# Kernel optimization log

Hardware: AMD Instinct MI355X
Metric: run time of the kernel (lower is better)

Reference implementation:

```python
import jax, jax.numpy as jnp
import numpy as np

TAU = 2.0
V_TH = 1.0
V_RESET = 0.0
BN_EPS = 1e-5
SG_ALPHA = 2.0  # spikingjelly ATan surrogate default

@jax.custom_vjp
def spike_fn(x):
    return (x >= 0.0).astype(x.dtype)

def _spike_fwd(x):
    return spike_fn(x), x

def _spike_bwd(x, g):
    # ATan surrogate: alpha/2 / (1 + (pi/2*alpha*x)^2)
    sg = (SG_ALPHA / 2.0) / (1.0 + (jnp.pi / 2.0 * SG_ALPHA * x) ** 2)
    return (g * sg,)

spike_fn.defvjp(_spike_fwd, _spike_bwd)

def lif_multistep(x_seq):
    # x_seq: [T, B, C]; decay_input=False, hard reset, detach_reset=True
    def step(v, xt):
        v = v - (v - V_RESET) / TAU + xt
        s = spike_fn(v - V_TH)
        sd = jax.lax.stop_gradient(s)
        v = (1.0 - sd) * v + sd * V_RESET
        return v, s
    v0 = jnp.zeros_like(x_seq[0])
    _, s_seq = jax.lax.scan(step, v0, x_seq)
    return s_seq

def bn_eval(x, gamma, beta, mean, var):
    # x: [T, B, C], normalize over channel C (eval-mode BN)
    inv = gamma * jax.lax.rsqrt(var + BN_EPS)
    return x * inv + (beta - mean * inv)

def setup_inputs() -> dict:
    key = jax.random.key(0)
    ks = jax.random.split(key, 8)
    B, T, Cin, C, K = 64, 200, 80, 1024, 7
    x = jax.random.normal(ks[0], (B, T, Cin), dtype=jnp.float32)
    pw_w = jax.random.normal(ks[1], (C, Cin), dtype=jnp.float32) * (1.0 / np.sqrt(Cin))
    pw_b = jnp.zeros((C,), dtype=jnp.float32)
    dw_w = jax.random.normal(ks[2], (C, K), dtype=jnp.float32) * (1.0 / np.sqrt(K))
    dw_b = jnp.zeros((C,), dtype=jnp.float32)
    bn1_gamma = jnp.ones((C,), dtype=jnp.float32)
    bn1_beta = jnp.zeros((C,), dtype=jnp.float32)
    bn1_mean = jnp.zeros((C,), dtype=jnp.float32)
    bn1_var = jnp.ones((C,), dtype=jnp.float32)
    lin_w = jax.random.normal(ks[3], (C, C), dtype=jnp.float32) * (1.0 / np.sqrt(C))
    bn2_gamma = jnp.ones((C,), dtype=jnp.float32)
    bn2_beta = jnp.zeros((C,), dtype=jnp.float32)
    bn2_mean = jnp.zeros((C,), dtype=jnp.float32)
    bn2_var = jnp.ones((C,), dtype=jnp.float32)
    return dict(x=x, pw_w=pw_w, pw_b=pw_b, dw_w=dw_w, dw_b=dw_b,
                bn1_gamma=bn1_gamma, bn1_beta=bn1_beta, bn1_mean=bn1_mean, bn1_var=bn1_var,
                lin_w=lin_w,
                bn2_gamma=bn2_gamma, bn2_beta=bn2_beta, bn2_mean=bn2_mean, bn2_var=bn2_var)

def reference(x, pw_w, pw_b, dw_w, dw_b,
              bn1_gamma, bn1_beta, bn1_mean, bn1_var,
              lin_w,
              bn2_gamma, bn2_beta, bn2_mean, bn2_var):
    # x: [B, T, Cin] -> trans1 -> [B, Cin, T]
    h = jnp.transpose(x, (0, 2, 1))
    # pointwise conv1d (kernel 1): [B, Cin, T] -> [B, C, T]
    h = jnp.einsum('bct,oc->bot', h, pw_w) + pw_b[None, :, None]
    # depthwise conv1d, kernel 7, same padding
    C = dw_w.shape[0]
    h = jax.lax.conv_general_dilated(
        h, dw_w[:, None, :], window_strides=(1,), padding=[(3, 3)],
        feature_group_count=C, dimension_numbers=('NCH', 'OIH', 'NCH'))
    h = h + dw_b[None, :, None]
    # trans2: [B, C, T] -> [T, B, C]
    h = jnp.transpose(h, (2, 0, 1))
    h = bn_eval(h, bn1_gamma, bn1_beta, bn1_mean, bn1_var)
    h = lif_multistep(h)
    # dropout1: eval mode -> identity
    h_res = h
    h = jnp.einsum('tbc,oc->tbo', h, lin_w)  # Linear, no bias
    h = bn_eval(h, bn2_gamma, bn2_beta, bn2_mean, bn2_var)
    h = lif_multistep(h)
    # dropout2: eval mode -> identity
    return h + h_res  # [T, B, C]
```

## Files before the change

kernel.cpp:

```cpp
#include <hip/hip_runtime.h>
#include <hip/hip_bf16.h>
#include <stdint.h>

#define B_    64
#define T_    200
#define CIN_  80
#define C_    1024
#define M_    (B_ * T_)
#define BCEL  (B_ * C_)

typedef __attribute__((ext_vector_type(4))) float f32x4;
typedef __attribute__((ext_vector_type(8))) _Float16 f16x8;
typedef __attribute__((ext_vector_type(4))) unsigned int u32x4;

__global__ __launch_bounds__(256) void gemm_abt128(
    const float* __restrict__ A, const float* __restrict__ Bm,
    const float* __restrict__ bias, float* __restrict__ C,
    int M, int N, int K) {
  __shared__ float As[16][128];
  __shared__ float Bs[16][128];
  const int tid = threadIdx.x;
  const int tx = tid & 15;
  const int ty = tid >> 4;
  const int m0 = blockIdx.x * 128;
  const int n0 = blockIdx.y * 128;
  const int lr = tid >> 1;
  const int lc = (tid & 1) * 8;

  float acc[8][8] = {};

  const float* Ar = A + (size_t)(m0 + lr) * K + lc;
  const float* Br = Bm + (size_t)(n0 + lr) * K + lc;

  float4 a0 = *(const float4*)(Ar + 0);
  float4 a1 = *(const float4*)(Ar + 4);
  float4 b0 = *(const float4*)(Br + 0);
  float4 b1 = *(const float4*)(Br + 4);

  for (int k0 = 0; k0 < K; k0 += 16) {
    __syncthreads();
    As[lc + 0][lr] = a0.x; As[lc + 1][lr] = a0.y;
    As[lc + 2][lr] = a0.z; As[lc + 3][lr] = a0.w;
    As[lc + 4][lr] = a1.x; As[lc + 5][lr] = a1.y;
    As[lc + 6][lr] = a1.z; As[lc + 7][lr] = a1.w;
    Bs[lc + 0][lr] = b0.x; Bs[lc + 1][lr] = b0.y;
    Bs[lc + 2][lr] = b0.z; Bs[lc + 3][lr] = b0.w;
    Bs[lc + 4][lr] = b1.x; Bs[lc + 5][lr] = b1.y;
    Bs[lc + 6][lr] = b1.z; Bs[lc + 7][lr] = b1.w;
    __syncthreads();
    if (k0 + 16 < K) {
      a0 = *(const float4*)(Ar + k0 + 16);
      a1 = *(const float4*)(Ar + k0 + 20);
      b0 = *(const float4*)(Br + k0 + 16);
      b1 = *(const float4*)(Br + k0 + 20);
    }
#pragma unroll
    for (int kk = 0; kk < 16; ++kk) {
      float4 av0 = *(const float4*)&As[kk][ty * 4];
      float4 av1 = *(const float4*)&As[kk][ty * 4 + 64];
      float4 bv0 = *(const float4*)&Bs[kk][tx * 4];
      float4 bv1 = *(const float4*)&Bs[kk][tx * 4 + 64];
      float avv[8] = {av0.x, av0.y, av0.z, av0.w, av1.x, av1.y, av1.z, av1.w};
      float bvv[8] = {bv0.x, bv0.y, bv0.z, bv0.w, bv1.x, bv1.y, bv1.z, bv1.w};
#pragma unroll
      for (int i = 0; i < 8; ++i)
#pragma unroll
        for (int j = 0; j < 8; ++j)
          acc[i][j] = fmaf(avv[i], bvv[j], acc[i][j]);
    }
  }

  float bj[8] = {0.f, 0.f, 0.f, 0.f, 0.f, 0.f, 0.f, 0.f};
  if (bias) {
#pragma unroll
    for (int j = 0; j < 8; ++j)
      bj[j] = bias[n0 + tx * 4 + (j & 3) + (j >> 2) * 64];
  }
#pragma unroll
  for (int i = 0; i < 8; ++i) {
    int row = m0 + ty * 4 + (i & 3) + (i >> 2) * 64;
    float4 o0, o1;
    o0.x = acc[i][0] + bj[0]; o0.y = acc[i][1] + bj[1];
    o0.z = acc[i][2] + bj[2]; o0.w = acc[i][3] + bj[3];
    o1.x = acc[i][4] + bj[4]; o1.y = acc[i][5] + bj[5];
    o1.z = acc[i][6] + bj[6]; o1.w = acc[i][7] + bj[7];
    *(float4*)&C[(size_t)row * N + n0 + tx * 4] = o0;
    *(float4*)&C[(size_t)row * N + n0 + tx * 4 + 64] = o1;
  }
}

__global__ __launch_bounds__(256) void dw_bn_lif(
    const float* __restrict__ p, const float* __restrict__ dw_w,
    const float* __restrict__ dw_b, const float* __restrict__ gam,
    const float* __restrict__ bet, const float* __restrict__ mu,
    const float* __restrict__ var, ushort* __restrict__ s1) {
  int gid = blockIdx.x * blockDim.x + threadIdx.x;
  int b = gid >> 10;
  int o = gid & 1023;

  float w[7];
#pragma unroll
  for (int k = 0; k < 7; ++k) w[k] = dw_w[o * 7 + k];
  float db = dw_b[o];
  float inv = (float)((double)gam[o] / sqrt((double)var[o] + 1e-5));
  float add = (float)((double)bet[o] - (double)mu[o] * (double)inv);

  const float* pp = p + (size_t)b * T_ * C_ + o;
  float win[14];
  win[0] = 0.f; win[1] = 0.f; win[2] = 0.f;
#pragma unroll
  for (int i = 0; i < 11; ++i) win[3 + i] = pp[(size_t)i * C_];

  float v = 0.f;
  size_t obase = (size_t)b * C_ + o;
  for (int c = 0; c < T_ / 8; ++c) {
    int t0 = c * 8;
    float nx[8];
#pragma unroll
    for (int j = 0; j < 8; ++j) {
      int tn = t0 + 11 + j;
      nx[j] = (tn < T_) ? pp[(size_t)tn * C_] : 0.f;
    }
#pragma unroll
    for (int s = 0; s < 8; ++s) {
      float u = db;
#pragma unroll
      for (int k = 0; k < 7; ++k) u = fmaf(w[k], win[s + k], u);
      u = fmaf(u, inv, add);
      v = fmaf(0.5f, v, u);
      bool sp = (v - 1.0f) >= 0.0f;
      s1[obase + (size_t)(t0 + s) * BCEL] = sp ? (ushort)0x3C00 : (ushort)0;
      v = sp ? 0.0f : v;
    }
#pragma unroll
    for (int i = 0; i < 6; ++i) win[i] = win[i + 8];
#pragma unroll
    for (int j = 0; j < 8; ++j) win[6 + j] = nx[j];
  }
}

__global__ __launch_bounds__(256) void split_w(
    const float* __restrict__ w, ushort* __restrict__ w0,
    ushort* __restrict__ w1, int n) {
  int i = blockIdx.x * 256 + threadIdx.x;
  if (i >= n) return;
  float x = w[i];
  union { _Float16 h; ushort u; } h0, h1;
  h0.h = (_Float16)x;
  if (fabsf(x) < 6.1035156e-5f) h0.u = 0;
  float r = x - (float)h0.h;
  h1.h = (_Float16)(r * 2048.0f);
  w0[i] = h0.u;
  w1[i] = h1.u;
}

#define GBM 256
#define GBN 256
#define GBK 32
#define NKT (C_ / GBK)

__global__ __launch_bounds__(512, 2) void gemm_mfma8p(
    const ushort* __restrict__ A,
    const ushort* __restrict__ B0,
    const ushort* __restrict__ B1,
    float* __restrict__ Cout) {
  const int K = C_;
  const int N = C_;
  __shared__ ushort lds8[3][3][GBM * GBK];

  const int tid  = threadIdx.x;
  const int lane = tid & 63;
  const int wid  = tid >> 6;
  const int wm = (wid >> 2) * 128;
  const int wn = (wid & 3) * 64;

  int lin = blockIdx.x;
  int wg  = (lin & 7) * 25 + (lin >> 3);
  const int m0 = (wg >> 2) * GBM;
  const int n0 = (wg & 3) * GBN;

  const int ar0 = tid >> 2, ar1 = ar0 + 128;
  const int aks = ((tid & 3) * 8) ^ (((tid >> 3) & 3) << 3);

  const int fr  = lane & 15;
  const int k8s = ((lane >> 4) * 8) ^ (((fr >> 1) & 3) << 3);

  f32x4 acc[8][4] = {};

#define STG(MATP, RB, MI, SLOT, K0S)                                           \
  do {                                                                         \
    __builtin_amdgcn_global_load_lds(                                          \
        (const __attribute__((address_space(1))) uint32_t*)((MATP) + (size_t)((RB) + ar0) * K + (K0S) + aks), \
        (__attribute__((address_space(3))) uint32_t*)&lds8[SLOT][MI][tid * 8], 16, 0, 0);                     \
    __builtin_amdgcn_global_load_lds(                                          \
        (const __attribute__((address_space(1))) uint32_t*)((MATP) + (size_t)((RB) + ar1) * K + (K0S) + aks), \
        (__attribute__((address_space(3))) uint32_t*)&lds8[SLOT][MI][(tid + 512) * 8], 16, 0, 0);             \
  } while (0)

#define NOSTG ((void)0)
#define VM6 asm volatile("s_waitcnt vmcnt(6)" ::: "memory")

#define PHASE(Q, SRD, STAGE_STMT, VMSTMT)                                      \
  do {                                                                         \
    constexpr int FRB = ((Q) & 1) * 4;                                         \
    constexpr int FCB = ((Q) >> 1) * 2;                                        \
    const ushort* As_  = &lds8[SRD][0][0];                                     \
    const ushort* B0s_ = &lds8[SRD][1][0];                                     \
    const ushort* B1s_ = &lds8[SRD][2][0];                                     \
    f16x8 a0_ = *(const f16x8*)&As_[(wm + (FRB + 0) * 16 + fr) * GBK + k8s];   \
    f16x8 a1_ = *(const f16x8*)&As_[(wm + (FRB + 1) * 16 + fr) * GBK + k8s];   \
    f16x8 a2_ = *(const f16x8*)&As_[(wm + (FRB + 2) * 16 + fr) * GBK + k8s];   \
    f16x8 a3_ = *(const f16x8*)&As_[(wm + (FRB + 3) * 16 + fr) * GBK + k8s];   \
    f16x8 p0_ = *(const f16x8*)&B0s_[(wn + (FCB + 0) * 16 + fr) * GBK + k8s];  \
    f16x8 p1_ = *(const f16x8*)&B0s_[(wn + (FCB + 1) * 16 + fr) * GBK + k8s];  \
    f16x8 q0_ = *(const f16x8*)&B1s_[(wn + (FCB + 0) * 16 + fr) * GBK + k8s];  \
    f16x8 q1_ = *(const f16x8*)&B1s_[(wn + (FCB + 1) * 16 + fr) * GBK + k8s];  \
    STAGE_STMT;                                                                \
    __builtin_amdgcn_s_barrier();                                              \
    asm volatile("s_waitcnt lgkmcnt(0)" ::: "memory");                         \
    __builtin_amdgcn_s_setprio(1);                                             \
    union HU_ { f16x8 h; u32x4 u; };                                           \
    HU_ x0_, x1_, x2_, x3_;                                                    \
    x0_.h = a0_; x0_.u &= 0x10001000u;                                         \
    x1_.h = a1_; x1_.u &= 0x10001000u;                                         \
    x2_.h = a2_; x2_.u &= 0x10001000u;                                         \
    x3_.h = a3_; x3_.u &= 0x10001000u;                                         \
    acc[FRB + 0][FCB + 0] = __builtin_amdgcn_mfma_f32_16x16x32_f16(a0_, p0_, acc[FRB + 0][FCB + 0], 0, 0, 0); \
    acc[FRB + 0][FCB + 0] = __builtin_amdgcn_mfma_f32_16x16x32_f16(x0_.h, q0_, acc[FRB + 0][FCB + 0], 0, 0, 0); \
    acc[FRB + 1][FCB + 0] = __builtin_amdgcn_mfma_f32_16x16x32_f16(a1_, p0_, acc[FRB + 1][FCB + 0], 0, 0, 0); \
    acc[FRB + 1][FCB + 0] = __builtin_amdgcn_mfma_f32_16x16x32_f16(x1_.h, q0_, acc[FRB + 1][FCB + 0], 0, 0, 0); \
    acc[FRB + 2][FCB + 0] = __builtin_amdgcn_mfma_f32_16x16x32_f16(a2_, p0_, acc[FRB + 2][FCB + 0], 0, 0, 0); \
    acc[FRB + 2][FCB + 0] = __builtin_amdgcn_mfma_f32_16x16x32_f16(x2_.h, q0_, acc[FRB + 2][FCB + 0], 0, 0, 0); \
    acc[FRB + 3][FCB + 0] = __builtin_amdgcn_mfma_f32_16x16x32_f16(a3_, p0_, acc[FRB + 3][FCB + 0], 0, 0, 0); \
    acc[FRB + 3][FCB + 0] = __builtin_amdgcn_mfma_f32_16x16x32_f16(x3_.h, q0_, acc[FRB + 3][FCB + 0], 0, 0, 0); \
    acc[FRB + 0][FCB + 1] = __builtin_amdgcn_mfma_f32_16x16x32_f16(a0_, p1_, acc[FRB + 0][FCB + 1], 0, 0, 0); \
    acc[FRB + 0][FCB + 1] = __builtin_amdgcn_mfma_f32_16x16x32_f16(x0_.h, q1_, acc[FRB + 0][FCB + 1], 0, 0, 0); \
    acc[FRB + 1][FCB + 1] = __builtin_amdgcn_mfma_f32_16x16x32_f16(a1_, p1_, acc[FRB + 1][FCB + 1], 0, 0, 0); \
    acc[FRB + 1][FCB + 1] = __builtin_amdgcn_mfma_f32_16x16x32_f16(x1_.h, q1_, acc[FRB + 1][FCB + 1], 0, 0, 0); \
    acc[FRB + 2][FCB + 1] = __builtin_amdgcn_mfma_f32_16x16x32_f16(a2_, p1_, acc[FRB + 2][FCB + 1], 0, 0, 0); \
    acc[FRB + 2][FCB + 1] = __builtin_amdgcn_mfma_f32_16x16x32_f16(x2_.h, q1_, acc[FRB + 2][FCB + 1], 0, 0, 0); \
    acc[FRB + 3][FCB + 1] = __builtin_amdgcn_mfma_f32_16x16x32_f16(a3_, p1_, acc[FRB + 3][FCB + 1], 0, 0, 0); \
    acc[FRB + 3][FCB + 1] = __builtin_amdgcn_mfma_f32_16x16x32_f16(x3_.h, q1_, acc[FRB + 3][FCB + 1], 0, 0, 0); \
    __builtin_amdgcn_s_setprio(0);                                             \
    VMSTMT;                                                                    \
    __builtin_amdgcn_s_barrier();                                              \
  } while (0)

  STG(A, m0, 0, 0, 0);  STG(B0, n0, 1, 0, 0);  STG(B1, n0, 2, 0, 0);
  STG(A, m0, 0, 1, GBK); STG(B0, n0, 1, 1, GBK); STG(B1, n0, 2, 1, GBK);
  asm volatile("s_waitcnt vmcnt(6)" ::: "memory");
  __builtin_amdgcn_s_barrier();

  int s0 = 0;
  for (int it = 0; it < NKT / 2; ++it) {
    const int t0 = 2 * it;
    int s1 = s0 + 1; if (s1 == 3) s1 = 0;
    int s2 = s1 + 1; if (s2 == 3) s2 = 0;
    const int ka = (t0 + 2 < NKT) ? (t0 + 2) * GBK : 0;
    const int kb = (t0 + 3 < NKT) ? (t0 + 3) * GBK : 0;
    PHASE(0, s0, STG(A,  m0, 0, s2, ka), NOSTG);
    PHASE(1, s0, STG(B0, n0, 1, s2, ka), NOSTG);
    PHASE(2, s0, STG(B1, n0, 2, s2, ka), NOSTG);
    PHASE(3, s0, NOSTG, VM6);
    PHASE(0, s1, STG(A,  m0, 0, s0, kb), NOSTG);
    PHASE(1, s1, STG(B0, n0, 1, s0, kb), NOSTG);
    PHASE(2, s1, STG(B1, n0, 2, s0, kb), NOSTG);
    PHASE(3, s1, NOSTG, VM6);
    s0 = s2;
  }
#undef PHASE
#undef STG

  const int ccol = lane & 15;
  const int crow = (lane >> 4) * 4;
#pragma unroll
  for (int m = 0; m < 8; ++m)
#pragma unroll
    for (int n = 0; n < 4; ++n)
#pragma unroll
      for (int j = 0; j < 4; ++j) {
        int row = m0 + wm + m * 16 + crow + j;
        int col = n0 + wn + n * 16 + ccol;
        Cout[(size_t)row * N + col] = acc[m][n][j];
      }
}

__global__ __launch_bounds__(256) void bn_lif_add(
    const float* __restrict__ y, const ushort* __restrict__ s1b,
    const float* __restrict__ gam, const float* __restrict__ bet,
    const float* __restrict__ mu, const float* __restrict__ var,
    float* __restrict__ out) {
  int gid = blockIdx.x * blockDim.x + threadIdx.x;
  int o = gid & 1023;

  float inv = (float)((double)gam[o] / sqrt((double)var[o] + 1e-5));
  float add = (float)((double)bet[o] - (double)mu[o] * (double)inv);

  float v = 0.f;
  size_t base = (size_t)gid;
  float yv[8]; ushort sv[8];
#pragma unroll
  for (int j = 0; j < 8; ++j) {
    yv[j] = y[base + (size_t)j * BCEL];
    sv[j] = s1b[base + (size_t)j * BCEL];
  }
  for (int c = 0; c < T_ / 8; ++c) {
    int t0 = c * 8;
    float yn[8] = {0,0,0,0,0,0,0,0}; ushort sn[8] = {0,0,0,0,0,0,0,0};
    if (c + 1 < T_ / 8) {
#pragma unroll
      for (int j = 0; j < 8; ++j) {
        size_t idx = base + (size_t)(t0 + 8 + j) * BCEL;
        yn[j] = y[idx];
        sn[j] = s1b[idx];
      }
    }
#pragma unroll
    for (int j = 0; j < 8; ++j) {
      float u = fmaf(yv[j], inv, add);
      v = fmaf(0.5f, v, u);
      bool sp = (v - 1.0f) >= 0.0f;
      float s1v = sv[j] ? 1.0f : 0.0f;
      out[base + (size_t)(t0 + j) * BCEL] = (sp ? 1.0f : 0.0f) + s1v;
      v = sp ? 0.0f : v;
    }
#pragma unroll
    for (int j = 0; j < 8; ++j) { yv[j] = yn[j]; sv[j] = sn[j]; }
  }
}

extern "C" void kernel_launch(void* const* d_in, const int* in_sizes, int n_in,
                              void* d_out, int out_size, void* d_ws,
                              size_t ws_size, hipStream_t stream) {
  const float* x     = (const float*)d_in[0];
  const float* pw_w  = (const float*)d_in[1];
  const float* pw_b  = (const float*)d_in[2];
  const float* dw_w  = (const float*)d_in[3];
  const float* dw_b  = (const float*)d_in[4];
  const float* bn1g  = (const float*)d_in[5];
  const float* bn1b  = (const float*)d_in[6];
  const float* bn1m  = (const float*)d_in[7];
  const float* bn1v  = (const float*)d_in[8];
  const float* lin_w = (const float*)d_in[9];
  const float* bn2g  = (const float*)d_in[10];
  const float* bn2b  = (const float*)d_in[11];
  const float* bn2m  = (const float*)d_in[12];
  const float* bn2v  = (const float*)d_in[13];

  char* wsb  = (char*)d_ws;
  char* outb = (char*)d_out;
  const size_t PB  = (size_t)M_ * C_ * 4;
  const size_t SBB = (size_t)M_ * C_ * 2;

  float* p = (float*)d_ws;

  const bool primary = ws_size >= PB + SBB;
  ushort* spikes = primary ? (ushort*)(wsb + PB) : (ushort*)d_out;
  ushort* w0  = primary ? (ushort*)outb : (ushort*)(wsb + SBB);
  ushort* w1s = w0 + (size_t)C_ * C_;
  ushort* Sgemm = primary ? spikes : (ushort*)d_ws;
  float* ybuf = primary ? (float*)d_ws : (float*)d_out;

  dim3 pw_grid(M_ / 128, C_ / 128);
  gemm_abt128<<<pw_grid, 256, 0, stream>>>(x, pw_w, pw_b, p, M_, C_, CIN_);

  dw_bn_lif<<<BCEL / 256, 256, 0, stream>>>(p, dw_w, dw_b, bn1g, bn1b, bn1m,
                                            bn1v, spikes);

  if (!primary)
    hipMemcpyAsync(d_ws, d_out, SBB, hipMemcpyDeviceToDevice, stream);

  split_w<<<(C_ * C_ + 255) / 256, 256, 0, stream>>>(lin_w, w0, w1s, C_ * C_);

  gemm_mfma8p<<<(M_ / GBM) * (C_ / GBN), 512, 0, stream>>>(Sgemm, w0, w1s,
                                                           ybuf);

  bn_lif_add<<<BCEL / 256, 256, 0, stream>>>(ybuf, Sgemm, bn2g, bn2b, bn2m,
                                             bn2v, (float*)d_out);
}
```

Baseline: 147.4 us.

## Switch main GEMM to 32x32x16 MFMA and fuse weight split into pointwise GEMM

The main spike-by-weight GEMM now uses 32x32x16 f16 MFMA instructions with 4x2 accumulator tiles in place of 16x16x32 tiles. This changes the LDS fragment addressing, the swizzle and the output store layout. The larger MFMA shape is meant to reduce instruction count and LDS fragment traffic per flop. Separately, the fp16 hi/lo weight split is folded into the pointwise-conv GEMM launch as extra blocks, which removes one kernel launch and lets the split run alongside that GEMM. The new swizzle has to match the global_load_lds staging pattern, and the larger accumulators raise register pressure.

Result: no change. 150.1 us (+1.8%).

```diff
diff --git a/kernel.cpp b/kernel.cpp
--- a/kernel.cpp
+++ b/kernel.cpp
@@ -9,26 +9,49 @@
 #define M_    (B_ * T_)
 #define BCEL  (B_ * C_)
 
-typedef __attribute__((ext_vector_type(4))) float f32x4;
-typedef __attribute__((ext_vector_type(8))) _Float16 f16x8;
-typedef __attribute__((ext_vector_type(4))) unsigned int u32x4;
-
-__global__ __launch_bounds__(256) void gemm_abt128(
+typedef __attribute__((ext_vector_type(4)))  float f32x4;
+typedef __attribute__((ext_vector_type(16))) float f32x16;
+typedef __attribute__((ext_vector_type(8)))  _Float16 f16x8;
+typedef __attribute__((ext_vector_type(4)))  unsigned int u32x4;
+
+__global__ __launch_bounds__(256) void pw_and_split(
     const float* __restrict__ A, const float* __restrict__ Bm,
     const float* __restrict__ bias, float* __restrict__ C,
-    int M, int N, int K) {
+    const float* __restrict__ lw, ushort* __restrict__ w0,
+    ushort* __restrict__ w1, int M, int N, int K) {
   __shared__ float As[16][128];
   __shared__ float Bs[16][128];
+  const int bx = blockIdx.x;
   const int tid = threadIdx.x;
+
+  if (bx >= 800) {
+    int base = ((bx - 800) * 256 + tid) * 4;
+    float4 xv = *(const float4*)(lw + base);
+    float xs[4] = {xv.x, xv.y, xv.z, xv.w};
+    ushort o0[4], o1[4];
+#pragma unroll
+    for (int j = 0; j < 4; ++j) {
+      float x = xs[j];
+      union { _Float16 h; ushort u; } h0, h1;
+      h0.h = (_Float16)x;
+      if (fabsf(x) < 6.1035156e-5f) h0.u = 0;
+      float r = x - (float)h0.h;
+      h1.h = (_Float16)(r * 2048.0f);
+      o0[j] = h0.u; o1[j] = h1.u;
+    }
+    *(ushort4*)(w0 + base) = make_ushort4(o0[0], o0[1], o0[2], o0[3]);
+    *(ushort4*)(w1 + base) = make_ushort4(o1[0], o1[1], o1[2], o1[3]);
+    return;
+  }
+
   const int tx = tid & 15;
   const int ty = tid >> 4;
-  const int m0 = blockIdx.x * 128;
-  const int n0 = blockIdx.y * 128;
+  const int m0 = (bx % 100) * 128;
+  const int n0 = (bx / 100) * 128;
   const int lr = tid >> 1;
   const int lc = (tid & 1) * 8;
 
   float acc[8][8] = {};
-
   const float* Ar = A + (size_t)(m0 + lr) * K + lc;
   const float* Br = Bm + (size_t)(n0 + lr) * K + lc;
 
@@ -71,11 +94,9 @@
   }
 
   float bj[8] = {0.f, 0.f, 0.f, 0.f, 0.f, 0.f, 0.f, 0.f};
-  if (bias) {
-#pragma unroll
-    for (int j = 0; j < 8; ++j)
-      bj[j] = bias[n0 + tx * 4 + (j & 3) + (j >> 2) * 64];
-  }
+#pragma unroll
+  for (int j = 0; j < 8; ++j)
+    bj[j] = bias[n0 + tx * 4 + (j & 3) + (j >> 2) * 64];
 #pragma unroll
   for (int i = 0; i < 8; ++i) {
     int row = m0 + ty * 4 + (i & 3) + (i >> 2) * 64;
@@ -139,27 +160,12 @@
   }
 }
 
-__global__ __launch_bounds__(256) void split_w(
-    const float* __restrict__ w, ushort* __restrict__ w0,
-    ushort* __restrict__ w1, int n) {
-  int i = blockIdx.x * 256 + threadIdx.x;
-  if (i >= n) return;
-  float x = w[i];
-  union { _Float16 h; ushort u; } h0, h1;
-  h0.h = (_Float16)x;
-  if (fabsf(x) < 6.1035156e-5f) h0.u = 0;
-  float r = x - (float)h0.h;
-  h1.h = (_Float16)(r * 2048.0f);
-  w0[i] = h0.u;
-  w1[i] = h1.u;
-}
-
 #define GBM 256
 #define GBN 256
 #define GBK 32
 #define NKT (C_ / GBK)
 
-__global__ __launch_bounds__(512, 2) void gemm_mfma8p(
+__global__ __launch_bounds__(512, 2) void gemm_mfma32(
     const ushort* __restrict__ A,
     const ushort* __restrict__ B0,
     const ushort* __restrict__ B1,
@@ -182,10 +188,11 @@
   const int ar0 = tid >> 2, ar1 = ar0 + 128;
   const int aks = ((tid & 3) * 8) ^ (((tid >> 3) & 3) << 3);
 
-  const int fr  = lane & 15;
-  const int k8s = ((lane >> 4) * 8) ^ (((fr >> 1) & 3) << 3);
-
-  f32x4 acc[8][4] = {};
+  const int l31 = lane & 31;
+  const int rsw = ((lane >> 1) & 3) << 3;
+  const int kb8 = (lane >> 5) * 8;
+
+  f32x16 acc[4][2] = {};
 
 #define STG(MATP, RB, MI, SLOT, K0S)                                           \
   do {                                                                         \
@@ -202,45 +209,43 @@
 
 #define PHASE(Q, SRD, STAGE_STMT, VMSTMT)                                      \
   do {                                                                         \
-    constexpr int FRB = ((Q) & 1) * 4;                                         \
-    constexpr int FCB = ((Q) >> 1) * 2;                                        \
+    constexpr int MB = ((Q) & 1) * 2;                                          \
+    constexpr int NB = ((Q) >> 1);                                             \
     const ushort* As_  = &lds8[SRD][0][0];                                     \
     const ushort* B0s_ = &lds8[SRD][1][0];                                     \
     const ushort* B1s_ = &lds8[SRD][2][0];                                     \
-    f16x8 a0_ = *(const f16x8*)&As_[(wm + (FRB + 0) * 16 + fr) * GBK + k8s];   \
-    f16x8 a1_ = *(const f16x8*)&As_[(wm + (FRB + 1) * 16 + fr) * GBK + k8s];   \
-    f16x8 a2_ = *(const f16x8*)&As_[(wm + (FRB + 2) * 16 + fr) * GBK + k8s];   \
-    f16x8 a3_ = *(const f16x8*)&As_[(wm + (FRB + 3) * 16 + fr) * GBK + k8s];   \
-    f16x8 p0_ = *(const f16x8*)&B0s_[(wn + (FCB + 0) * 16 + fr) * GBK + k8s];  \
-    f16x8 p1_ = *(const f16x8*)&B0s_[(wn + (FCB + 1) * 16 + fr) * GBK + k8s];  \
-    f16x8 q0_ = *(const f16x8*)&B1s_[(wn + (FCB + 0) * 16 + fr) * GBK + k8s];  \
-    f16x8 q1_ = *(const f16x8*)&B1s_[(wn + (FCB + 1) * 16 + fr) * GBK + k8s];  \
+    f16x8 aa[2][2], bb0[2], bb1[2];                                            \
+    _Pragma("unroll")                                                          \
+    for (int mb = 0; mb < 2; ++mb)                                             \
+      _Pragma("unroll")                                                        \
+      for (int kc = 0; kc < 2; ++kc)                                           \
+        aa[mb][kc] = *(const f16x8*)&As_[(wm + (MB + mb) * 32 + l31) * GBK +   \
+                                         ((kc * 16 + kb8) ^ rsw)];             \
+    _Pragma("unroll")                                                          \
+    for (int kc = 0; kc < 2; ++kc) {                                           \
+      bb0[kc] = *(const f16x8*)&B0s_[(wn + NB * 32 + l31) * GBK +              \
+                                     ((kc * 16 + kb8) ^ rsw)];                 \
+      bb1[kc] = *(const f16x8*)&B1s_[(wn + NB * 32 + l31) * GBK +              \
+                                     ((kc * 16 + kb8) ^ rsw)];                 \
+    }                                                                          \
     STAGE_STMT;                                                                \
     __builtin_amdgcn_s_barrier();                                              \
     asm volatile("s_waitcnt lgkmcnt(0)" ::: "memory");                         \
     __builtin_amdgcn_s_setprio(1);                                             \
     union HU_ { f16x8 h; u32x4 u; };                                           \
-    HU_ x0_, x1_, x2_, x3_;                                                    \
-    x0_.h = a0_; x0_.u &= 0x10001000u;                                         \
-    x1_.h = a1_; x1_.u &= 0x10001000u;                                         \
-    x2_.h = a2_; x2_.u &= 0x10001000u;                                         \
-    x3_.h = a3_; x3_.u &= 0x10001000u;                                         \
-    acc[FRB + 0][FCB + 0] = __builtin_amdgcn_mfma_f32_16x16x32_f16(a0_, p0_, acc[FRB + 0][FCB + 0], 0, 0, 0); \
-    acc[FRB + 0][FCB + 0] = __builtin_amdgcn_mfma_f32_16x16x32_f16(x0_.h, q0_, acc[FRB + 0][FCB + 0], 0, 0, 0); \
-    acc[FRB + 1][FCB + 0] = __builtin_amdgcn_mfma_f32_16x16x32_f16(a1_, p0_, acc[FRB + 1][FCB + 0], 0, 0, 0); \
-    acc[FRB + 1][FCB + 0] = __builtin_amdgcn_mfma_f32_16x16x32_f16(x1_.h, q0_, acc[FRB + 1][FCB + 0], 0, 0, 0); \
-    acc[FRB + 2][FCB + 0] = __builtin_amdgcn_mfma_f32_16x16x32_f16(a2_, p0_, acc[FRB + 2][FCB + 0], 0, 0, 0); \
-    acc[FRB + 2][FCB + 0] = __builtin_amdgcn_mfma_f32_16x16x32_f16(x2_.h, q0_, acc[FRB + 2][FCB + 0], 0, 0, 0); \
-    acc[FRB + 3][FCB + 0] = __builtin_amdgcn_mfma_f32_16x16x32_f16(a3_, p0_, acc[FRB + 3][FCB + 0], 0, 0, 0); \
-    acc[FRB + 3][FCB + 0] = __builtin_amdgcn_mfma_f32_16x16x32_f16(x3_.h, q0_, acc[FRB + 3][FCB + 0], 0, 0, 0); \
-    acc[FRB + 0][FCB + 1] = __builtin_amdgcn_mfma_f32_16x16x32_f16(a0_, p1_, acc[FRB + 0][FCB + 1], 0, 0, 0); \
-    acc[FRB + 0][FCB + 1] = __builtin_amdgcn_mfma_f32_16x16x32_f16(x0_.h, q1_, acc[FRB + 0][FCB + 1], 0, 0, 0); \
-    acc[FRB + 1][FCB + 1] = __builtin_amdgcn_mfma_f32_16x16x32_f16(a1_, p1_, acc[FRB + 1][FCB + 1], 0, 0, 0); \
-    acc[FRB + 1][FCB + 1] = __builtin_amdgcn_mfma_f32_16x16x32_f16(x1_.h, q1_, acc[FRB + 1][FCB + 1], 0, 0, 0); \
-    acc[FRB + 2][FCB + 1] = __builtin_amdgcn_mfma_f32_16x16x32_f16(a2_, p1_, acc[FRB + 2][FCB + 1], 0, 0, 0); \
-    acc[FRB + 2][FCB + 1] = __builtin_amdgcn_mfma_f32_16x16x32_f16(x2_.h, q1_, acc[FRB + 2][FCB + 1], 0, 0, 0); \
-    acc[FRB + 3][FCB + 1] = __builtin_amdgcn_mfma_f32_16x16x32_f16(a3_, p1_, acc[FRB + 3][FCB + 1], 0, 0, 0); \
-    acc[FRB + 3][FCB + 1] = __builtin_amdgcn_mfma_f32_16x16x32_f16(x3_.h, q1_, acc[FRB + 3][FCB + 1], 0, 0, 0); \
+    _Pragma("unroll")                                                          \
+    for (int mb = 0; mb < 2; ++mb) {                                           \
+      _Pragma("unroll")                                                        \
+      for (int kc = 0; kc < 2; ++kc) {                                         \
+        HU_ xm_;                                                               \
+        xm_.h = aa[mb][kc];                                                    \
+        xm_.u &= 0x10001000u;             \
+        acc[MB + mb][NB] = __builtin_amdgcn_mfma_f32_32x32x16_f16(             \
+            aa[mb][kc], bb0[kc], acc[MB + mb][NB], 0, 0, 0);                   \
+        acc[MB + mb][NB] = __builtin_amdgcn_mfma_f32_32x32x16_f16(             \
+            xm_.h, bb1[kc], acc[MB + mb][NB], 0, 0, 0);                        \
+      }                                                                        \
+    }                                                                          \
     __builtin_amdgcn_s_setprio(0);                                             \
     VMSTMT;                                                                    \
     __builtin_amdgcn_s_barrier();                                              \
@@ -271,17 +276,16 @@
 #undef PHASE
 #undef STG
 
-  const int ccol = lane & 15;
-  const int crow = (lane >> 4) * 4;
-#pragma unroll
-  for (int m = 0; m < 8; ++m)
-#pragma unroll
-    for (int n = 0; n < 4; ++n)
-#pragma unroll
-      for (int j = 0; j < 4; ++j) {
-        int row = m0 + wm + m * 16 + crow + j;
-        int col = n0 + wn + n * 16 + ccol;
-        Cout[(size_t)row * N + col] = acc[m][n][j];
+  const int rbase = (lane >> 5) * 4;
+#pragma unroll
+  for (int mb = 0; mb < 4; ++mb)
+#pragma unroll
+    for (int nb = 0; nb < 2; ++nb)
+#pragma unroll
+      for (int rg = 0; rg < 16; ++rg) {
+        int row = m0 + wm + mb * 32 + (rg & 3) + 8 * (rg >> 2) + rbase;
+        int col = n0 + wn + nb * 32 + l31;
+        Cout[(size_t)row * N + col] = acc[mb][nb][rg];
       }
 }
 
@@ -361,8 +365,8 @@
   ushort* Sgemm = primary ? spikes : (ushort*)d_ws;
   float* ybuf = primary ? (float*)d_ws : (float*)d_out;
 
-  dim3 pw_grid(M_ / 128, C_ / 128);
-  gemm_abt128<<<pw_grid, 256, 0, stream>>>(x, pw_w, pw_b, p, M_, C_, CIN_);
+  pw_and_split<<<800 + 1024, 256, 0, stream>>>(x, pw_w, pw_b, p, lin_w, w0,
+                                               w1s, M_, C_, CIN_);
 
   dw_bn_lif<<<BCEL / 256, 256, 0, stream>>>(p, dw_w, dw_b, bn1g, bn1b, bn1m,
                                             bn1v, spikes);
@@ -370,9 +374,7 @@
   if (!primary)
     hipMemcpyAsync(d_ws, d_out, SBB, hipMemcpyDeviceToDevice, stream);
 
-  split_w<<<(C_ * C_ + 255) / 256, 256, 0, stream>>>(lin_w, w0, w1s, C_ * C_);
-
-  gemm_mfma8p<<<(M_ / GBM) * (C_ / GBN), 512, 0, stream>>>(Sgemm, w0, w1s,
+  gemm_mfma32<<<(M_ / GBM) * (C_ / GBN), 512, 0, stream>>>(Sgemm, w0, w1s,
                                                            ybuf);
 
   bn_lif_add<<<BCEL / 256, 256, 0, stream>>>(ybuf, Sgemm, bn2g, bn2b, bn2m,
```
